# Performance work log

Hardware: AMD Instinct MI355X
Metric: run time of the kernel (lower is better)

The kernel has to match this reference:

```python
import jax, jax.numpy as jnp
from jax import lax
import numpy as np

K = 3          # sampling grid size (kernel_size)
WS = 4         # scope kernel size (weight_shape)
DILATION = 1


def setup_inputs() -> dict:
    key = jax.random.key(0)
    k1, k2, k3, k4 = jax.random.split(key, 4)
    x = jax.random.normal(k1, (4, 128, 56, 56), jnp.float32)
    # offset conv is zero-initialized in the original; use small values so offsets are realistic
    offset_w = jax.random.normal(k2, (2 * K * K, 128, K, K), jnp.float32) * 0.01
    offset_b = jax.random.normal(k3, (2 * K * K,), jnp.float32) * 0.01
    weight = jax.random.normal(k4, (128, WS, WS), jnp.float32) * 0.1  # depthwise scope kernel
    return {"x": x, "offset_w": offset_w, "offset_b": offset_b, "weight": weight}


def reference(x, offset_w, offset_b, weight):
    B, C, H, W = x.shape
    K2 = K * K
    # offset conv: 3x3, stride 1, pad 1 (same geometry as main conv)
    off = lax.conv_general_dilated(
        x, offset_w, window_strides=(1, 1), padding=[(1, 1), (1, 1)],
        dimension_numbers=("NCHW", "OIHW", "NCHW"))
    off = off + offset_b[None, :, None, None]
    off = off * DILATION                     # offset_clip is None
    off = off.reshape(B, K2, 2, H, W)
    dy, dx = off[:, :, 0], off[:, :, 1]      # [B,K2,H,W]

    # base coordinates of the KxK sampling grid centered inside the WSxWS scope kernel
    base = jnp.arange(K, dtype=x.dtype) - (K - 1) / 2 + (WS - 1) / 2   # [K]
    by = jnp.repeat(base, K)                 # k = i*K + j -> row i
    bx = jnp.tile(base, K)                   # k = i*K + j -> col j
    yc = dy + by[None, :, None, None]        # [B,K2,H,W] sampling coords in kernel space
    xc = dx + bx[None, :, None, None]

    # bilinear sampling of the scope kernel (zero outside scope)
    wflat = weight.reshape(C, WS * WS)
    y0 = jnp.floor(yc)
    x0 = jnp.floor(xc)
    samp = jnp.zeros((C, B, K2, H, W), x.dtype)
    for oy, ox in ((0, 0), (0, 1), (1, 0), (1, 1)):
        yi = y0 + oy
        xi = x0 + ox
        coef = (1.0 - jnp.abs(yc - yi)) * (1.0 - jnp.abs(xc - xi))
        valid = (yi >= 0) & (yi < WS) & (xi >= 0) & (xi < WS)
        idx = (jnp.clip(yi, 0, WS - 1) * WS + jnp.clip(xi, 0, WS - 1)).astype(jnp.int32)
        vals = jnp.take(wflat, idx, axis=1)  # [C,B,K2,H,W] irregular gather
        samp = samp + (coef * valid)[None] * vals
    samp = jnp.moveaxis(samp, 0, 1)          # [B,C,K2,H,W]

    # depthwise conv with per-pixel sampled kernels (stride 1, pad 1, dilation 1)
    xp = jnp.pad(x, ((0, 0), (0, 0), (1, 1), (1, 1)))
    pats = jnp.stack([xp[:, :, i:i + H, j:j + W] for i in range(K) for j in range(K)], axis=2)
    return jnp.sum(samp * pats, axis=2)      # [B,C,H,W]
```

## Files before the change

### kernel.cpp

```cpp
#include <hip/hip_runtime.h>

#define CC 128
#define HH 56
#define WW 56
#define NK2 9
#define NO 18
#define WSZ 4
#define W64 64

typedef __attribute__((ext_vector_type(8))) short short8;
typedef __attribute__((ext_vector_type(4))) float f32x4;

#define WSW_SHORTS  (9L * 2 * 4 * 64 * 8)
#define WSXB_SHORTS (4L * 58 * 58 * 128)
#define WSC_ENTRIES (4L * NK2 * HH * W64)

__device__ __forceinline__ unsigned short f2bf(float f) {
    unsigned u = __builtin_bit_cast(unsigned, f);
    u = u + 0x7fffu + ((u >> 16) & 1u);
    return (unsigned short)(u >> 16);
}

__global__ __launch_bounds__(256) void prep(
    const float* __restrict__ x,
    const float* __restrict__ offset_w,
    unsigned short* __restrict__ xb,
    unsigned short* __restrict__ wsW)
{
    const int blk = blockIdx.x;
    const int t   = threadIdx.x;
    if (blk < 232) {
        const int b  = blk / 58;
        const int hp = blk - b * 58;
        const int h  = hp - 1;
        __shared__ unsigned short s[CC][58];
        if (h >= 0 && h < HH) {
            for (int i = t; i < CC * WW; i += 256) {
                const int c = i / WW, w = i - c * WW;
                s[c][w + 1] = f2bf(x[(((long)b * CC + c) * HH + h) * WW + w]);
            }
        }
        __syncthreads();
        for (int j = t; j < 58 * CC; j += 256) {
            const int wp = j >> 7, c = j & 127;
            unsigned short v = 0;
            if (h >= 0 && h < HH && wp >= 1 && wp <= WW) v = s[c][wp];
            xb[(((long)b * 58 + hp) * 58 + wp) * CC + c] = v;
        }
    } else {
        const int e = (blk - 232) * 256 + t;
        if (e >= (int)WSW_SHORTS) return;
        const int j    = e & 7;
        const int lane = (e >> 3) & 63;
        const int kt   = (e >> 9) & 3;
        const int mt   = (e >> 11) & 1;
        const int k9   = e >> 12;
        const int o = mt * 16 + (lane & 15);
        const int c = kt * 32 + (lane >> 4) * 8 + j;
        float v = 0.f;
        if (o < NO) v = offset_w[(o * CC + c) * 9 + k9];
        wsW[e] = f2bf(v);
    }
}

__global__ __launch_bounds__(1024) void conv_mfma(
    const unsigned short* __restrict__ xb,
    const unsigned short* __restrict__ wsW,
    const float* __restrict__ offset_b,
    float4* __restrict__ wsC,
    unsigned* __restrict__ wsI)
{
    const int blk = blockIdx.x;
    const int b = blk / HH;
    const int h = blk - b * HH;
    const int t = threadIdx.x;
    const int lane = t & 63;
    const int wv = t >> 6;

    __shared__ float s_red[2][NO][W64];

    const int nt  = wv & 3;
    const int mt  = (wv >> 2) & 1;
    const int kh  = wv >> 3;
    const int q   = lane >> 4;
    const int n15 = lane & 15;

    f32x4 acc = {0.f, 0.f, 0.f, 0.f};
    const int k9lo = kh ? 5 : 0;
    const int k9hi = kh ? 9 : 5;
    for (int k9 = k9lo; k9 < k9hi; ++k9) {
        const int ky = k9 / 3, kx = k9 - ky * 3;
        int col = nt * 16 + n15 + kx;
        col = col > 57 ? 57 : col;
        const unsigned short* bbase =
            xb + (((long)b * 58 + (h + ky)) * 58 + col) * CC + q * 8;
        const unsigned short* abase =
            wsW + ((long)(k9 * 2 + mt) * 4 * 64 + lane) * 8;
        #pragma unroll
        for (int kt = 0; kt < 4; ++kt) {
            short8 a  = *(const short8*)(abase + kt * 512);
            short8 bf = *(const short8*)(bbase + kt * 32);
            acc = __builtin_amdgcn_mfma_f32_16x16x32_bf16(a, bf, acc, 0, 0, 0);
        }
    }
    #pragma unroll
    for (int reg = 0; reg < 4; ++reg) {
        const int o = mt * 16 + q * 4 + reg;
        if (o < NO) s_red[kh][o][nt * 16 + n15] = acc[reg];
    }
    __syncthreads();

    if (t < NK2 * 64) {
        const int k2 = t >> 6;
        const int px = t & 63;
        const float dy = s_red[0][2 * k2][px] + s_red[1][2 * k2][px]
                       + offset_b[2 * k2];
        const float dx = s_red[0][2 * k2 + 1][px] + s_red[1][2 * k2 + 1][px]
                       + offset_b[2 * k2 + 1];
        const float yc = dy + 0.5f + (float)(k2 / 3);
        const float xc = dx + 0.5f + (float)(k2 % 3);
        const float y0 = floorf(yc), x0f = floorf(xc);
        const float fy = yc - y0, fx = xc - x0f;
        const int yi = (int)y0, xi = (int)x0f;
        float cf[4]; int id[4];
        #pragma unroll
        for (int qq = 0; qq < 4; ++qq) {
            const int oy = qq >> 1, ox = qq & 1;
            const int yy = yi + oy, xx = xi + ox;
            float c2 = (oy ? fy : 1.f - fy) * (ox ? fx : 1.f - fx);
            const bool valid = (yy >= 0) && (yy < WSZ) && (xx >= 0) && (xx < WSZ);
            cf[qq] = valid ? c2 : 0.f;
            const int yyc = yy < 0 ? 0 : (yy > 3 ? 3 : yy);
            const int xxc = xx < 0 ? 0 : (xx > 3 ? 3 : xx);
            id[qq] = yyc * 4 + xxc;
        }
        const long oidx = ((long)(b * NK2 + k2) * HH + h) * W64 + px;
        wsC[oidx] = make_float4(cf[0], cf[1], cf[2], cf[3]);
        wsI[oidx] = (unsigned)(id[0] | (id[1] << 4) | (id[2] << 8) | (id[3] << 12));
    }
}

__global__ __launch_bounds__(128) void sample_kernel(
    const float* __restrict__ x,
    const float* __restrict__ weight,
    const float4* __restrict__ wsC,
    const unsigned* __restrict__ wsI,
    float* __restrict__ out)
{
    const int blk = blockIdx.x;
    const int bh  = blk >> 4;
    const int cg  = blk & 15;
    const int b   = bh / HH;
    const int h   = bh - b * HH;
    const int t   = threadIdx.x;
    const int lane = t & 63;
    const int wv  = __builtin_amdgcn_readfirstlane(t >> 6);

    __shared__ float s_wT[16][12];
    if (t < 128) {
        const int j = t >> 3, cl = t & 7;
        s_wT[j][cl] = weight[(cg * 8 + cl) * 16 + j];
    }
    __syncthreads();

    if (lane >= WW) return;
    const int w = lane;
    const int cl0 = wv * 4;

    float4 cf[NK2]; unsigned pk[NK2];
    const long cidx0 = ((long)b * NK2 * HH + h) * W64 + w;
    #pragma unroll
    for (int k2 = 0; k2 < NK2; ++k2) {
        cf[k2] = wsC[cidx0 + (long)k2 * HH * W64];
        pk[k2] = wsI[cidx0 + (long)k2 * HH * W64];
    }

    float xv[4][9];
    #pragma unroll
    for (int u = 0; u < 4; ++u) {
        const int c = cg * 8 + cl0 + u;
        const float* xc = x + ((long)b * CC + c) * HH * WW;
        #pragma unroll
        for (int ky = 0; ky < 3; ++ky) {
            const int hy = h + ky - 1;
            #pragma unroll
            for (int kx = 0; kx < 3; ++kx) {
                const int wx = w + kx - 1;
                float v = 0.f;
                if (hy >= 0 && hy < HH && wx >= 0 && wx < WW)
                    v = xc[hy * WW + wx];
                xv[u][ky * 3 + kx] = v;
            }
        }
    }

    float res[4] = {0.f, 0.f, 0.f, 0.f};
    #pragma unroll
    for (int k2 = 0; k2 < NK2; ++k2) {
        const unsigned p = pk[k2];
        const float4 W0 = *(const float4*)&s_wT[p & 15][cl0];
        const float4 W1 = *(const float4*)&s_wT[(p >> 4) & 15][cl0];
        const float4 W2 = *(const float4*)&s_wT[(p >> 8) & 15][cl0];
        const float4 W3 = *(const float4*)&s_wT[(p >> 12) & 15][cl0];
        const float4 c4 = cf[k2];
        res[0] += (c4.x * W0.x + c4.y * W1.x + c4.z * W2.x + c4.w * W3.x) * xv[0][k2];
        res[1] += (c4.x * W0.y + c4.y * W1.y + c4.z * W2.y + c4.w * W3.y) * xv[1][k2];
        res[2] += (c4.x * W0.z + c4.y * W1.z + c4.z * W2.z + c4.w * W3.z) * xv[2][k2];
        res[3] += (c4.x * W0.w + c4.y * W1.w + c4.z * W2.w + c4.w * W3.w) * xv[3][k2];
    }

    #pragma unroll
    for (int u = 0; u < 4; ++u) {
        const int c = cg * 8 + cl0 + u;
        out[(((long)b * CC + c) * HH + h) * WW + w] = res[u];
    }
}

extern "C" void kernel_launch(void* const* d_in, const int* in_sizes, int n_in,
                              void* d_out, int out_size, void* d_ws, size_t ws_size,
                              hipStream_t stream) {
    const float* x        = (const float*)d_in[0];
    const float* offset_w = (const float*)d_in[1];
    const float* offset_b = (const float*)d_in[2];
    const float* weight   = (const float*)d_in[3];
    float* out = (float*)d_out;

    char* p = (char*)d_ws;
    unsigned short* wsW = (unsigned short*)p;           p += WSW_SHORTS * 2;
    unsigned short* xb  = (unsigned short*)p;           p += WSXB_SHORTS * 2;
    float4*         wsC = (float4*)p;                   p += WSC_ENTRIES * 16;
    unsigned*       wsI = (unsigned*)p;

    prep         <<<232 + 144, 256, 0, stream>>>(x, offset_w, xb, wsW);
    conv_mfma    <<<4 * HH, 1024, 0, stream>>>(xb, wsW, offset_b, wsC, wsI);
    sample_kernel<<<224 * 16, 128, 0, stream>>>(x, weight, wsC, wsI, out);
}
```

Baseline: 91.61 us.

## Fuse offset conv and sampling into one kernel using shared-memory coefficients

```diff
diff --git a/kernel.cpp b/kernel.cpp
--- a/kernel.cpp
+++ b/kernel.cpp
@@ -13,7 +13,6 @@
 
 #define WSW_SHORTS  (9L * 2 * 4 * 64 * 8)
 #define WSXB_SHORTS (4L * 58 * 58 * 128)
-#define WSC_ENTRIES (4L * NK2 * HH * W64)
 
 __device__ __forceinline__ unsigned short f2bf(float f) {
     unsigned u = __builtin_bit_cast(unsigned, f);
@@ -63,12 +62,13 @@
     }
 }
 
-__global__ __launch_bounds__(1024) void conv_mfma(
+__global__ __launch_bounds__(1024) void conv_sample(
+    const float* __restrict__ x,
     const unsigned short* __restrict__ xb,
     const unsigned short* __restrict__ wsW,
     const float* __restrict__ offset_b,
-    float4* __restrict__ wsC,
-    unsigned* __restrict__ wsI)
+    const float* __restrict__ weight,
+    float* __restrict__ out)
 {
     const int blk = blockIdx.x;
     const int b = blk / HH;
@@ -77,7 +77,15 @@
     const int lane = t & 63;
     const int wv = t >> 6;
 
-    __shared__ float s_red[2][NO][W64];
+    __shared__ float    s_red[2][NO][W64];
+    __shared__ float    s_cf[4][NK2][W64];
+    __shared__ unsigned s_id[NK2][W64];
+    __shared__ float    s_wT[16][132];
+
+    for (int i = t; i < 16 * CC; i += 1024) {
+        const int c = i >> 4, j = i & 15;
+        s_wT[j][c] = weight[c * 16 + j];
+    }
 
     const int nt  = wv & 3;
     const int mt  = (wv >> 2) & 1;
@@ -134,85 +142,61 @@
             const int xxc = xx < 0 ? 0 : (xx > 3 ? 3 : xx);
             id[qq] = yyc * 4 + xxc;
         }
-        const long oidx = ((long)(b * NK2 + k2) * HH + h) * W64 + px;
-        wsC[oidx] = make_float4(cf[0], cf[1], cf[2], cf[3]);
-        wsI[oidx] = (unsigned)(id[0] | (id[1] << 4) | (id[2] << 8) | (id[3] << 12));
-    }
-}
-
-__global__ __launch_bounds__(128) void sample_kernel(
-    const float* __restrict__ x,
-    const float* __restrict__ weight,
-    const float4* __restrict__ wsC,
-    const unsigned* __restrict__ wsI,
-    float* __restrict__ out)
-{
-    const int blk = blockIdx.x;
-    const int bh  = blk >> 4;
-    const int cg  = blk & 15;
-    const int b   = bh / HH;
-    const int h   = bh - b * HH;
-    const int t   = threadIdx.x;
-    const int lane = t & 63;
-    const int wv  = __builtin_amdgcn_readfirstlane(t >> 6);
-
-    __shared__ float s_wT[16][12];
-    if (t < 128) {
-        const int j = t >> 3, cl = t & 7;
-        s_wT[j][cl] = weight[(cg * 8 + cl) * 16 + j];
+        s_cf[0][k2][px] = cf[0];
+        s_cf[1][k2][px] = cf[1];
+        s_cf[2][k2][px] = cf[2];
+        s_cf[3][k2][px] = cf[3];
+        s_id[k2][px] = (unsigned)(id[0] | (id[1] << 4) | (id[2] << 8) | (id[3] << 12));
     }
     __syncthreads();
 
-    if (lane >= WW) return;
-    const int w = lane;
-    const int cl0 = wv * 4;
-
-    float4 cf[NK2]; unsigned pk[NK2];
-    const long cidx0 = ((long)b * NK2 * HH + h) * W64 + w;
-    #pragma unroll
-    for (int k2 = 0; k2 < NK2; ++k2) {
-        cf[k2] = wsC[cidx0 + (long)k2 * HH * W64];
-        pk[k2] = wsI[cidx0 + (long)k2 * HH * W64];
-    }
-
-    float xv[4][9];
-    #pragma unroll
-    for (int u = 0; u < 4; ++u) {
-        const int c = cg * 8 + cl0 + u;
-        const float* xc = x + ((long)b * CC + c) * HH * WW;
+    if (lane < WW) {
+        const int px = lane;
+        const int c0 = __builtin_amdgcn_readfirstlane(wv) * 8;
         #pragma unroll
-        for (int ky = 0; ky < 3; ++ky) {
-            const int hy = h + ky - 1;
+        for (int sub = 0; sub < 2; ++sub) {
+            const int cb = c0 + sub * 4;
+            float xv[4][9];
             #pragma unroll
-            for (int kx = 0; kx < 3; ++kx) {
-                const int wx = w + kx - 1;
-                float v = 0.f;
-                if (hy >= 0 && hy < HH && wx >= 0 && wx < WW)
-                    v = xc[hy * WW + wx];
-                xv[u][ky * 3 + kx] = v;
-            }
-        }
-    }
-
-    float res[4] = {0.f, 0.f, 0.f, 0.f};
-    #pragma unroll
-    for (int k2 = 0; k2 < NK2; ++k2) {
-        const unsigned p = pk[k2];
-        const float4 W0 = *(const float4*)&s_wT[p & 15][cl0];
-        const float4 W1 = *(const float4*)&s_wT[(p >> 4) & 15][cl0];
-        const float4 W2 = *(const float4*)&s_wT[(p >> 8) & 15][cl0];
-        const float4 W3 = *(const float4*)&s_wT[(p >> 12) & 15][cl0];
-        const float4 c4 = cf[k2];
-        res[0] += (c4.x * W0.x + c4.y * W1.x + c4.z * W2.x + c4.w * W3.x) * xv[0][k2];
-        res[1] += (c4.x * W0.y + c4.y * W1.y + c4.z * W2.y + c4.w * W3.y) * xv[1][k2];
-        res[2] += (c4.x * W0.z + c4.y * W1.z + c4.z * W2.z + c4.w * W3.z) * xv[2][k2];
-        res[3] += (c4.x * W0.w + c4.y * W1.w + c4.z * W2.w + c4.w * W3.w) * xv[3][k2];
-    }
-
-    #pragma unroll
-    for (int u = 0; u < 4; ++u) {
-        const int c = cg * 8 + cl0 + u;
-        out[(((long)b * CC + c) * HH + h) * WW + w] = res[u];
+            for (int u = 0; u < 4; ++u) {
+                const int c = cb + u;
+                const float* xc = x + ((long)b * CC + c) * HH * WW;
+                #pragma unroll
+                for (int ky = 0; ky < 3; ++ky) {
+                    const int hy = h + ky - 1;
+                    #pragma unroll
+                    for (int kx = 0; kx < 3; ++kx) {
+                        const int wx = px + kx - 1;
+                        float v = 0.f;
+                        if (hy >= 0 && hy < HH && wx >= 0 && wx < WW)
+                            v = xc[hy * WW + wx];
+                        xv[u][ky * 3 + kx] = v;
+                    }
+                }
+            }
+            float res[4] = {0.f, 0.f, 0.f, 0.f};
+            #pragma unroll
+            for (int k2 = 0; k2 < NK2; ++k2) {
+                const unsigned p = s_id[k2][px];
+                const float c0f = s_cf[0][k2][px];
+                const float c1f = s_cf[1][k2][px];
+                const float c2f = s_cf[2][k2][px];
+                const float c3f = s_cf[3][k2][px];
+                const float4 W0 = *(const float4*)&s_wT[p & 15][cb];
+                const float4 W1 = *(const float4*)&s_wT[(p >> 4) & 15][cb];
+                const float4 W2 = *(const float4*)&s_wT[(p >> 8) & 15][cb];
+                const float4 W3 = *(const float4*)&s_wT[(p >> 12) & 15][cb];
+                res[0] += (c0f * W0.x + c1f * W1.x + c2f * W2.x + c3f * W3.x) * xv[0][k2];
+                res[1] += (c0f * W0.y + c1f * W1.y + c2f * W2.y + c3f * W3.y) * xv[1][k2];
+                res[2] += (c0f * W0.z + c1f * W1.z + c2f * W2.z + c3f * W3.z) * xv[2][k2];
+                res[3] += (c0f * W0.w + c1f * W1.w + c2f * W2.w + c3f * W3.w) * xv[3][k2];
+            }
+            #pragma unroll
+            for (int u = 0; u < 4; ++u) {
+                const int c = cb + u;
+                out[(((long)b * CC + c) * HH + h) * WW + px] = res[u];
+            }
+        }
     }
 }
 
@@ -227,11 +211,8 @@
 
     char* p = (char*)d_ws;
     unsigned short* wsW = (unsigned short*)p;           p += WSW_SHORTS * 2;
-    unsigned short* xb  = (unsigned short*)p;           p += WSXB_SHORTS * 2;
-    float4*         wsC = (float4*)p;                   p += WSC_ENTRIES * 16;
-    unsigned*       wsI = (unsigned*)p;
-
-    prep         <<<232 + 144, 256, 0, stream>>>(x, offset_w, xb, wsW);
-    conv_mfma    <<<4 * HH, 1024, 0, stream>>>(xb, wsW, offset_b, wsC, wsI);
-    sample_kernel<<<224 * 16, 128, 0, stream>>>(x, weight, wsC, wsI, out);
-}
+    unsigned short* xb  = (unsigned short*)p;
+
+    prep       <<<232 + 144, 256, 0, stream>>>(x, offset_w, xb, wsW);
+    conv_sample<<<4 * HH, 1024, 0, stream>>>(x, xb, wsW, offset_b, weight, out);
+}
```

After: 89.76 us, median of 2. 1.02x faster.
